# Performance work log

Measured on AMD Instinct MI355X. Metric: run time of the kernel, lower is better.

Reference implementation:

```python
import jax, jax.numpy as jnp
import numpy as np

S, B, H = 2048, 32, 1024

def setup_inputs() -> dict:
    key = jax.random.key(0)
    k1, k2, k3, k4, k5 = jax.random.split(key, 5)
    stdv = 1.0 / np.sqrt(2 * H)  # nn.Linear default init scale (approx, uniform in torch)
    return {
        "hidden": jax.random.normal(k1, (1, B, H), dtype=jnp.float32),
        "encoder_outputs": jax.random.normal(k2, (S, B, H), dtype=jnp.float32),
        "W": jax.random.normal(k3, (H, 2 * H), dtype=jnp.float32) * stdv,
        "b": jax.random.normal(k4, (H,), dtype=jnp.float32) * stdv,
        "v": jax.random.normal(k5, (H,), dtype=jnp.float32) * (1.0 / np.sqrt(H)),
    }

def reference(hidden, encoder_outputs, W, b, v):
    # hidden: (1, B, H); encoder_outputs: (S, B, H)
    h = hidden[0]                              # (B, H)
    e = jnp.swapaxes(encoder_outputs, 0, 1)    # (B, S, H)
    Wh, We = W[:, :H], W[:, H:]                # split concat-linear: cat([H_rep, enc]) @ W^T
    # energy = tanh(Linear(cat([H, enc], -1)))  -> (B, S, H)
    pre_h = h @ Wh.T                           # (B, H), broadcast over S (H is repeated per step)
    pre_e = jnp.einsum('bsh,kh->bsk', e, We)   # (B, S, H)
    energy = jnp.tanh(pre_e + pre_h[:, None, :] + b)
    scores = jnp.einsum('bsk,k->bs', energy, v)  # v-dot per position -> (B, S)
    return jax.nn.softmax(scores, axis=1)[:, None, :]  # (B, 1, S)
```

## Files before the change

kernel.cpp:

```cpp
#include <hip/hip_runtime.h>


#define LDA 72

typedef __attribute__((ext_vector_type(8))) short short8;
typedef __attribute__((ext_vector_type(4))) float floatx4;
typedef __attribute__((ext_vector_type(4))) unsigned int uint4v;

#define GLDS(g, l) __builtin_amdgcn_global_load_lds( \
    (const __attribute__((address_space(1))) void*)(g), \
    (__attribute__((address_space(3))) void*)(l), 16, 0, 0)

__device__ __forceinline__ unsigned short f2b(float f) {
  union { float f; unsigned u; } c; c.f = f;
  unsigned r = c.u + 0x7fffu + ((c.u >> 16) & 1u);
  return (unsigned short)(r >> 16);
}

__device__ __forceinline__ unsigned pack2(float lo, float hi) {
  union { float f; unsigned u; } a, b; a.f = lo; b.f = hi;
  return __builtin_amdgcn_perm(b.u + 0x8000u, a.u + 0x8000u, 0x07060302u);
}

__device__ __forceinline__ float fast_tanh(float x) {
  float e = __expf(2.0f * x);
  return 1.0f - 2.0f / (e + 1.0f);
}

__global__ __launch_bounds__(256) void k_cvtB(
    const float* __restrict__ W, unsigned int* __restrict__ Bw2,
    float* __restrict__ scoresT) {
  const int idx = blockIdx.x * 256 + threadIdx.x;
  const int kc = idx >> 10, n = idx & 1023;
  const float* src = W + (size_t)n * 2048 + 1024 + kc * 8;
  float4 f0 = *(const float4*)(src);
  float4 f1 = *(const float4*)(src + 4);
  uint4v u = {pack2(f0.x, f0.y), pack2(f0.z, f0.w),
              pack2(f1.x, f1.y), pack2(f1.z, f1.w)};
  *(uint4v*)(Bw2 + ((size_t)kc * 8192 + n * 8) / 2) = u;
  if (idx < 65536) scoresT[idx] = 0.f;
}

__global__ __launch_bounds__(256) void k_preh(
    const float* __restrict__ hidden, const float* __restrict__ W,
    const float* __restrict__ bias, float* __restrict__ tpre) {
  const int g  = blockIdx.x * 256 + threadIdx.x;
  const int b  = g & 31;
  const int ko = g >> 5;
  const float* wr = W + (size_t)ko * 2048;
  const float* hr = hidden + b * 1024;
  float s = 0.f;
  #pragma unroll 8
  for (int j = 0; j < 1024; j += 4) {
    float4 wv = *(const float4*)(wr + j);
    float4 hv = *(const float4*)(hr + j);
    s += wv.x * hv.x + wv.y * hv.y + wv.z * hv.z + wv.w * hv.w;
  }
  tpre[b * 1024 + ko] = s + bias[ko];
}

__global__ __launch_bounds__(256, 4) void k_gemm(
    const float* __restrict__ A,
    const unsigned short* __restrict__ Bw2,
    const float* __restrict__ tpre,
    const float* __restrict__ vvec,
    float* __restrict__ scoresT) {
  __shared__ short As[64 * LDA];
  __shared__ short Bs[8 * 128 * 8];

  const int l = blockIdx.x;
  const int x = l & 7, j = l >> 3;
  const int Mbase = (x * 128 + (j >> 3)) * 64;
  const int Nbase = (j & 7) * 128;

  const int tid = threadIdx.x, lane = tid & 63, w = tid >> 6;
  const int wm = w >> 1, wn = w & 1;
  const int c = lane & 15, q = lane >> 4;

  const int arow = tid >> 2, acol = (tid & 3) << 4;
  const float* ap = A + (size_t)(Mbase + arow) * 1024 + acol;
  short* asw = &As[arow * LDA + acol];

  const unsigned short* bgb = Bw2 + (size_t)(Nbase + lane) * 8;

  floatx4 acc[2][4];
  #pragma unroll
  for (int mt = 0; mt < 2; ++mt)
    #pragma unroll
    for (int nt = 0; nt < 4; ++nt) {
      floatx4 z = {0.f, 0.f, 0.f, 0.f};
      acc[mt][nt] = z;
    }

  for (int k0 = 0; k0 < 1024; k0 += 64) {
    float4 g0 = *(const float4*)(ap + k0);
    float4 g1 = *(const float4*)(ap + k0 + 4);
    float4 g2 = *(const float4*)(ap + k0 + 8);
    float4 g3 = *(const float4*)(ap + k0 + 12);
    #pragma unroll
    for (int i = 0; i < 4; ++i) {
      const int seg = w * 4 + i;
      const int kcl = seg >> 1, half = seg & 1;
      GLDS(bgb + ((size_t)((k0 >> 3) + kcl) * 8192 + half * 512),
           &Bs[kcl * 1024 + half * 512]);
    }
    uint4v u0 = {pack2(g0.x, g0.y), pack2(g0.z, g0.w),
                 pack2(g1.x, g1.y), pack2(g1.z, g1.w)};
    uint4v u1 = {pack2(g2.x, g2.y), pack2(g2.z, g2.w),
                 pack2(g3.x, g3.y), pack2(g3.z, g3.w)};
    *(uint4v*)asw = u0;
    *(uint4v*)(asw + 8) = u1;
    __syncthreads();

    #pragma unroll
    for (int ks = 0; ks < 2; ++ks) {
      short8 af[2], bf[4];
      #pragma unroll
      for (int mt = 0; mt < 2; ++mt)
        af[mt] = *(const short8*)&As[(wm * 32 + mt * 16 + c) * LDA + ks * 32 + q * 8];
      #pragma unroll
      for (int nt = 0; nt < 4; ++nt)
        bf[nt] = *(const short8*)&Bs[(ks * 4 + q) * 1024 + (wn * 64 + nt * 16 + c) * 8];
      #pragma unroll
      for (int mt = 0; mt < 2; ++mt)
        #pragma unroll
        for (int nt = 0; nt < 4; ++nt)
          acc[mt][nt] = __builtin_amdgcn_mfma_f32_16x16x32_bf16(
              af[mt], bf[nt], acc[mt][nt], 0, 0, 0);
    }
    __syncthreads();
  }

  const int mwave = Mbase + wm * 32;
  const int nwave = Nbase + wn * 64;
  float vv[4];
  #pragma unroll
  for (int nt = 0; nt < 4; ++nt) vv[nt] = vvec[nwave + nt * 16 + c];
  #pragma unroll
  for (int mt = 0; mt < 2; ++mt) {
    #pragma unroll
    for (int i = 0; i < 4; ++i) {
      const int mrow = mwave + mt * 16 + q * 4 + i;
      const float* tb = tpre + (mrow & 31) * 1024;
      float ssum = 0.f;
      #pragma unroll
      for (int nt = 0; nt < 4; ++nt) {
        float pre = acc[mt][nt][i] + tb[nwave + nt * 16 + c];
        ssum += fast_tanh(pre) * vv[nt];
      }
      #pragma unroll
      for (int off = 1; off < 16; off <<= 1) ssum += __shfl_xor(ssum, off, 64);
      if (c == 0) atomicAdd(&scoresT[(mrow & 31) * 2048 + (mrow >> 5)], ssum);
    }
  }
}

__global__ __launch_bounds__(256) void k_softmax(
    const float* __restrict__ scoresT, float* __restrict__ out) {
  const int b = blockIdx.x;
  const int t = threadIdx.x;
  const int w = t >> 6, lane = t & 63;
  __shared__ float red[4];
  float vals[8];
  float m = -3.0e38f;
  #pragma unroll
  for (int i = 0; i < 8; ++i) {
    vals[i] = scoresT[b * 2048 + t + 256 * i];
    m = fmaxf(m, vals[i]);
  }
  #pragma unroll
  for (int off = 32; off; off >>= 1) m = fmaxf(m, __shfl_xor(m, off, 64));
  if (lane == 0) red[w] = m;
  __syncthreads();
  m = fmaxf(fmaxf(red[0], red[1]), fmaxf(red[2], red[3]));
  __syncthreads();
  float e[8];
  float sum = 0.f;
  #pragma unroll
  for (int i = 0; i < 8; ++i) { e[i] = __expf(vals[i] - m); sum += e[i]; }
  #pragma unroll
  for (int off = 32; off; off >>= 1) sum += __shfl_xor(sum, off, 64);
  if (lane == 0) red[w] = sum;
  __syncthreads();
  sum = red[0] + red[1] + red[2] + red[3];
  const float inv = 1.0f / sum;
  #pragma unroll
  for (int i = 0; i < 8; ++i) out[b * 2048 + t + 256 * i] = e[i] * inv;
}

extern "C" void kernel_launch(void* const* d_in, const int* in_sizes, int n_in,
                              void* d_out, int out_size, void* d_ws, size_t ws_size,
                              hipStream_t stream) {
  const float* hidden = (const float*)d_in[0];
  const float* enc    = (const float*)d_in[1];
  const float* W      = (const float*)d_in[2];
  const float* bias   = (const float*)d_in[3];
  const float* vvec   = (const float*)d_in[4];
  float* out = (float*)d_out;

  float* scoresT = (float*)d_ws;
  float* tpre    = scoresT + 65536;
  unsigned int* Bw2 = (unsigned int*)(tpre + 32768);

  hipLaunchKernelGGL(k_cvtB, dim3(512), dim3(256), 0, stream, W, Bw2, scoresT);
  hipLaunchKernelGGL(k_preh, dim3(128), dim3(256), 0, stream, hidden, W, bias, tpre);
  hipLaunchKernelGGL(k_gemm, dim3(8192), dim3(256), 0, stream,
                     enc, (const unsigned short*)Bw2, tpre, vvec, scoresT);
  hipLaunchKernelGGL(k_softmax, dim3(32), dim3(256), 0, stream, scoresT, out);
}
```

Before: 597.6 us.

## Double-buffer GEMM LDS tiles, enlarge M tile to 128, swizzle A layout

The GEMM kernel now computes a 128x128 tile per block instead of 64x128, halving the grid. It double-buffers both A and B in LDS so the next k-slice's global loads overlap the MFMA work on the current slice, with one barrier per iteration. The padded A layout is replaced by an XOR swizzle to avoid bank conflicts, and fp32-to-bf16 packing uses the hardware v_cvt_pk_bf16_f32 instruction. Doubled LDS use and more accumulator registers lower occupancy (launch bounds go from 4 to 2 blocks per CU).

After: 663.7 us. 11.1% more time.

```diff
diff --git a/kernel.cpp b/kernel.cpp
--- a/kernel.cpp
+++ b/kernel.cpp
@@ -1,7 +1,5 @@
 #include <hip/hip_runtime.h>
 
-
-#define LDA 72
 
 typedef __attribute__((ext_vector_type(8))) short short8;
 typedef __attribute__((ext_vector_type(4))) float floatx4;
@@ -11,15 +9,15 @@
     (const __attribute__((address_space(1))) void*)(g), \
     (__attribute__((address_space(3))) void*)(l), 16, 0, 0)
 
-__device__ __forceinline__ unsigned short f2b(float f) {
-  union { float f; unsigned u; } c; c.f = f;
-  unsigned r = c.u + 0x7fffu + ((c.u >> 16) & 1u);
-  return (unsigned short)(r >> 16);
-}
-
 __device__ __forceinline__ unsigned pack2(float lo, float hi) {
   union { float f; unsigned u; } a, b; a.f = lo; b.f = hi;
   return __builtin_amdgcn_perm(b.u + 0x8000u, a.u + 0x8000u, 0x07060302u);
+}
+
+__device__ __forceinline__ unsigned cvt_pk(float lo, float hi) {
+  unsigned r;
+  asm("v_cvt_pk_bf16_f32 %0, %1, %2" : "=v"(r) : "v"(lo), "v"(hi));
+  return r;
 }
 
 __device__ __forceinline__ float fast_tanh(float x) {
@@ -59,85 +57,136 @@
   tpre[b * 1024 + ko] = s + bias[ko];
 }
 
-__global__ __launch_bounds__(256, 4) void k_gemm(
+__device__ __forceinline__ void mma_tile(const short* __restrict__ Asb,
+                                         const short* __restrict__ Bsb,
+                                         int wm, int wn, int c, int q,
+                                         floatx4 acc[4][4]) {
+  #pragma unroll
+  for (int ks = 0; ks < 2; ++ks) {
+    short8 af[4], bf[4];
+    #pragma unroll
+    for (int mt = 0; mt < 4; ++mt) {
+      const int row = wm * 64 + mt * 16 + c;
+      af[mt] = *(const short8*)&Asb[row * 64 + (((ks * 4 + q) ^ (c & 7)) << 3)];
+    }
+    #pragma unroll
+    for (int nt = 0; nt < 4; ++nt)
+      bf[nt] = *(const short8*)&Bsb[(ks * 4 + q) * 1024 + (wn * 64 + nt * 16 + c) * 8];
+    #pragma unroll
+    for (int mt = 0; mt < 4; ++mt)
+      #pragma unroll
+      for (int nt = 0; nt < 4; ++nt)
+        acc[mt][nt] = __builtin_amdgcn_mfma_f32_16x16x32_bf16(
+            af[mt], bf[nt], acc[mt][nt], 0, 0, 0);
+  }
+}
+
+__global__ __launch_bounds__(256, 2) void k_gemm(
     const float* __restrict__ A,
     const unsigned short* __restrict__ Bw2,
     const float* __restrict__ tpre,
     const float* __restrict__ vvec,
     float* __restrict__ scoresT) {
-  __shared__ short As[64 * LDA];
-  __shared__ short Bs[8 * 128 * 8];
+  __shared__ short As[2][128 * 64];
+  __shared__ short Bs[2][8 * 128 * 8];
 
   const int l = blockIdx.x;
   const int x = l & 7, j = l >> 3;
-  const int Mbase = (x * 128 + (j >> 3)) * 64;
+  const int Mbase = (x * 64 + (j >> 3)) * 128;
   const int Nbase = (j & 7) * 128;
 
   const int tid = threadIdx.x, lane = tid & 63, w = tid >> 6;
   const int wm = w >> 1, wn = w & 1;
   const int c = lane & 15, q = lane >> 4;
 
-  const int arow = tid >> 2, acol = (tid & 3) << 4;
-  const float* ap = A + (size_t)(Mbase + arow) * 1024 + acol;
-  short* asw = &As[arow * LDA + acol];
+  const int arow  = tid >> 2;
+  const int ach   = (tid & 3) * 2;
+  const int acolF = (tid & 3) * 16;
+  const float* ap0 = A + (size_t)(Mbase + arow) * 1024 + acolF;
+  const float* ap1 = ap0 + 64 * 1024;
+  const int sw0 = (ach    ) ^ (arow & 7);
+  const int sw1 = (ach + 1) ^ (arow & 7);
 
   const unsigned short* bgb = Bw2 + (size_t)(Nbase + lane) * 8;
 
-  floatx4 acc[2][4];
-  #pragma unroll
-  for (int mt = 0; mt < 2; ++mt)
+  floatx4 acc[4][4];
+  #pragma unroll
+  for (int mt = 0; mt < 4; ++mt)
     #pragma unroll
     for (int nt = 0; nt < 4; ++nt) {
       floatx4 z = {0.f, 0.f, 0.f, 0.f};
       acc[mt][nt] = z;
     }
 
-  for (int k0 = 0; k0 < 1024; k0 += 64) {
-    float4 g0 = *(const float4*)(ap + k0);
-    float4 g1 = *(const float4*)(ap + k0 + 4);
-    float4 g2 = *(const float4*)(ap + k0 + 8);
-    float4 g3 = *(const float4*)(ap + k0 + 12);
+  {
+    float4 g[2][4];
+    #pragma unroll
+    for (int h = 0; h < 2; ++h) {
+      const float* ap = h ? ap1 : ap0;
+      #pragma unroll
+      for (int jj = 0; jj < 4; ++jj) g[h][jj] = *(const float4*)(ap + jj * 4);
+    }
     #pragma unroll
     for (int i = 0; i < 4; ++i) {
-      const int seg = w * 4 + i;
-      const int kcl = seg >> 1, half = seg & 1;
-      GLDS(bgb + ((size_t)((k0 >> 3) + kcl) * 8192 + half * 512),
-           &Bs[kcl * 1024 + half * 512]);
-    }
-    uint4v u0 = {pack2(g0.x, g0.y), pack2(g0.z, g0.w),
-                 pack2(g1.x, g1.y), pack2(g1.z, g1.w)};
-    uint4v u1 = {pack2(g2.x, g2.y), pack2(g2.z, g2.w),
-                 pack2(g3.x, g3.y), pack2(g3.z, g3.w)};
-    *(uint4v*)asw = u0;
-    *(uint4v*)(asw + 8) = u1;
+      const int seg = w * 4 + i, kcl = seg >> 1, half = seg & 1;
+      GLDS(bgb + ((size_t)kcl * 8192 + half * 512), &Bs[0][kcl * 1024 + half * 512]);
+    }
+    #pragma unroll
+    for (int h = 0; h < 2; ++h) {
+      short* base = &As[0][(arow + h * 64) * 64];
+      uint4v u0 = {cvt_pk(g[h][0].x, g[h][0].y), cvt_pk(g[h][0].z, g[h][0].w),
+                   cvt_pk(g[h][1].x, g[h][1].y), cvt_pk(g[h][1].z, g[h][1].w)};
+      uint4v u1 = {cvt_pk(g[h][2].x, g[h][2].y), cvt_pk(g[h][2].z, g[h][2].w),
+                   cvt_pk(g[h][3].x, g[h][3].y), cvt_pk(g[h][3].z, g[h][3].w)};
+      *(uint4v*)&base[sw0 << 3] = u0;
+      *(uint4v*)&base[sw1 << 3] = u1;
+    }
+  }
+  __syncthreads();
+
+  int cur = 0;
+  for (int t = 0; t < 15; ++t) {
+    const int nxt = cur ^ 1;
+    const int k1 = (t + 1) * 64;
+
+    float4 g[2][4];
+    #pragma unroll
+    for (int h = 0; h < 2; ++h) {
+      const float* ap = h ? ap1 : ap0;
+      #pragma unroll
+      for (int jj = 0; jj < 4; ++jj) g[h][jj] = *(const float4*)(ap + k1 + jj * 4);
+    }
+    #pragma unroll
+    for (int i = 0; i < 4; ++i) {
+      const int seg = w * 4 + i, kcl = seg >> 1, half = seg & 1;
+      GLDS(bgb + ((size_t)((k1 >> 3) + kcl) * 8192 + half * 512),
+           &Bs[nxt][kcl * 1024 + half * 512]);
+    }
+
+    mma_tile(&As[cur][0], &Bs[cur][0], wm, wn, c, q, acc);
+
+    #pragma unroll
+    for (int h = 0; h < 2; ++h) {
+      short* base = &As[nxt][(arow + h * 64) * 64];
+      uint4v u0 = {cvt_pk(g[h][0].x, g[h][0].y), cvt_pk(g[h][0].z, g[h][0].w),
+                   cvt_pk(g[h][1].x, g[h][1].y), cvt_pk(g[h][1].z, g[h][1].w)};
+      uint4v u1 = {cvt_pk(g[h][2].x, g[h][2].y), cvt_pk(g[h][2].z, g[h][2].w),
+                   cvt_pk(g[h][3].x, g[h][3].y), cvt_pk(g[h][3].z, g[h][3].w)};
+      *(uint4v*)&base[sw0 << 3] = u0;
+      *(uint4v*)&base[sw1 << 3] = u1;
+    }
     __syncthreads();
-
-    #pragma unroll
-    for (int ks = 0; ks < 2; ++ks) {
-      short8 af[2], bf[4];
-      #pragma unroll
-      for (int mt = 0; mt < 2; ++mt)
-        af[mt] = *(const short8*)&As[(wm * 32 + mt * 16 + c) * LDA + ks * 32 + q * 8];
-      #pragma unroll
-      for (int nt = 0; nt < 4; ++nt)
-        bf[nt] = *(const short8*)&Bs[(ks * 4 + q) * 1024 + (wn * 64 + nt * 16 + c) * 8];
-      #pragma unroll
-      for (int mt = 0; mt < 2; ++mt)
-        #pragma unroll
-        for (int nt = 0; nt < 4; ++nt)
-          acc[mt][nt] = __builtin_amdgcn_mfma_f32_16x16x32_bf16(
-              af[mt], bf[nt], acc[mt][nt], 0, 0, 0);
-    }
-    __syncthreads();
-  }
-
-  const int mwave = Mbase + wm * 32;
+    cur = nxt;
+  }
+  mma_tile(&As[cur][0], &Bs[cur][0], wm, wn, c, q, acc);
+
+  const int mwave = Mbase + wm * 64;
   const int nwave = Nbase + wn * 64;
   float vv[4];
   #pragma unroll
   for (int nt = 0; nt < 4; ++nt) vv[nt] = vvec[nwave + nt * 16 + c];
   #pragma unroll
-  for (int mt = 0; mt < 2; ++mt) {
+  for (int mt = 0; mt < 4; ++mt) {
     #pragma unroll
     for (int i = 0; i < 4; ++i) {
       const int mrow = mwave + mt * 16 + q * 4 + i;
@@ -204,7 +253,7 @@
 
   hipLaunchKernelGGL(k_cvtB, dim3(512), dim3(256), 0, stream, W, Bw2, scoresT);
   hipLaunchKernelGGL(k_preh, dim3(128), dim3(256), 0, stream, hidden, W, bias, tpre);
-  hipLaunchKernelGGL(k_gemm, dim3(8192), dim3(256), 0, stream,
+  hipLaunchKernelGGL(k_gemm, dim3(4096), dim3(256), 0, stream,
                      enc, (const unsigned short*)Bw2, tpre, vvec, scoresT);
   hipLaunchKernelGGL(k_softmax, dim3(32), dim3(256), 0, stream, scoresT, out);
 }
```

## Load fp32 A tile directly to LDS with swizzle, convert to bf16 at fragment read

Applied to the files above, without the earlier changes.

A-tile staging now goes straight from global memory to LDS in fp32 via global_load_lds, with an XOR swizzle on the column chunks to avoid bank conflicts. This replaces the old path of loading into registers, packing to bf16 and storing to LDS. Conversion to bf16 happens after the LDS read using the hardware v_cvt_pk_bf16_f32 instruction, and the launch-bounds occupancy hint rises from 4 to 5. The goal is to cut VGPR pressure and drop the register round-trip, at the cost of doubling A's LDS footprint and reading twice as many LDS bytes per fragment.

After: 609.4 us. Within noise of the previous version (+2.0%).

```diff
diff --git a/kernel.cpp b/kernel.cpp
--- a/kernel.cpp
+++ b/kernel.cpp
@@ -1,7 +1,5 @@
 #include <hip/hip_runtime.h>
 
-
-#define LDA 72
 
 typedef __attribute__((ext_vector_type(8))) short short8;
 typedef __attribute__((ext_vector_type(4))) float floatx4;
@@ -11,15 +9,15 @@
     (const __attribute__((address_space(1))) void*)(g), \
     (__attribute__((address_space(3))) void*)(l), 16, 0, 0)
 
-__device__ __forceinline__ unsigned short f2b(float f) {
-  union { float f; unsigned u; } c; c.f = f;
-  unsigned r = c.u + 0x7fffu + ((c.u >> 16) & 1u);
-  return (unsigned short)(r >> 16);
-}
-
 __device__ __forceinline__ unsigned pack2(float lo, float hi) {
   union { float f; unsigned u; } a, b; a.f = lo; b.f = hi;
   return __builtin_amdgcn_perm(b.u + 0x8000u, a.u + 0x8000u, 0x07060302u);
+}
+
+__device__ __forceinline__ unsigned cvt_pk(float lo, float hi) {
+  unsigned r;
+  asm("v_cvt_pk_bf16_f32 %0, %1, %2" : "=v"(r) : "v"(lo), "v"(hi));
+  return r;
 }
 
 __device__ __forceinline__ float fast_tanh(float x) {
@@ -59,13 +57,13 @@
   tpre[b * 1024 + ko] = s + bias[ko];
 }
 
-__global__ __launch_bounds__(256, 4) void k_gemm(
+__global__ __launch_bounds__(256, 5) void k_gemm(
     const float* __restrict__ A,
     const unsigned short* __restrict__ Bw2,
     const float* __restrict__ tpre,
     const float* __restrict__ vvec,
     float* __restrict__ scoresT) {
-  __shared__ short As[64 * LDA];
+  __shared__ float As[64 * 64];
   __shared__ short Bs[8 * 128 * 8];
 
   const int l = blockIdx.x;
@@ -77,9 +75,14 @@
   const int wm = w >> 1, wn = w & 1;
   const int c = lane & 15, q = lane >> 4;
 
-  const int arow = tid >> 2, acol = (tid & 3) << 4;
-  const float* ap = A + (size_t)(Mbase + arow) * 1024 + acol;
-  short* asw = &As[arow * LDA + acol];
+  const int rg = lane >> 4;
+  const float* aps[4];
+  #pragma unroll
+  for (int g = 0; g < 4; ++g) {
+    const int rlow = (g * 4 + rg) & 15;
+    const int schunk = (lane & 15) ^ rlow;
+    aps[g] = A + (size_t)(Mbase + w * 16 + g * 4 + rg) * 1024 + schunk * 4;
+  }
 
   const unsigned short* bgb = Bw2 + (size_t)(Nbase + lane) * 8;
 
@@ -93,31 +96,30 @@
     }
 
   for (int k0 = 0; k0 < 1024; k0 += 64) {
-    float4 g0 = *(const float4*)(ap + k0);
-    float4 g1 = *(const float4*)(ap + k0 + 4);
-    float4 g2 = *(const float4*)(ap + k0 + 8);
-    float4 g3 = *(const float4*)(ap + k0 + 12);
+    #pragma unroll
+    for (int g = 0; g < 4; ++g)
+      GLDS(aps[g] + k0, &As[(w * 16 + g * 4) * 64]);
     #pragma unroll
     for (int i = 0; i < 4; ++i) {
-      const int seg = w * 4 + i;
-      const int kcl = seg >> 1, half = seg & 1;
+      const int seg = w * 4 + i, kcl = seg >> 1, half = seg & 1;
       GLDS(bgb + ((size_t)((k0 >> 3) + kcl) * 8192 + half * 512),
            &Bs[kcl * 1024 + half * 512]);
     }
-    uint4v u0 = {pack2(g0.x, g0.y), pack2(g0.z, g0.w),
-                 pack2(g1.x, g1.y), pack2(g1.z, g1.w)};
-    uint4v u1 = {pack2(g2.x, g2.y), pack2(g2.z, g2.w),
-                 pack2(g3.x, g3.y), pack2(g3.z, g3.w)};
-    *(uint4v*)asw = u0;
-    *(uint4v*)(asw + 8) = u1;
     __syncthreads();
 
     #pragma unroll
     for (int ks = 0; ks < 2; ++ks) {
       short8 af[2], bf[4];
       #pragma unroll
-      for (int mt = 0; mt < 2; ++mt)
-        af[mt] = *(const short8*)&As[(wm * 32 + mt * 16 + c) * LDA + ks * 32 + q * 8];
+      for (int mt = 0; mt < 2; ++mt) {
+        const int r = wm * 32 + mt * 16 + c;
+        const int c0 = ks * 8 + q * 2;
+        const float4 lo = *(const float4*)&As[r * 64 + ((c0    ) ^ c) * 4];
+        const float4 hi = *(const float4*)&As[r * 64 + ((c0 + 1) ^ c) * 4];
+        uint4v ua = {cvt_pk(lo.x, lo.y), cvt_pk(lo.z, lo.w),
+                     cvt_pk(hi.x, hi.y), cvt_pk(hi.z, hi.w)};
+        af[mt] = *(short8*)&ua;
+      }
       #pragma unroll
       for (int nt = 0; nt < 4; ++nt)
         bf[nt] = *(const short8*)&Bs[(ks * 4 + q) * 1024 + (wn * 64 + nt * 16 + c) * 8];
```
